# Kernel optimization log

Measured on AMD Instinct MI355X. Metric: run time of the kernel, lower is better.

Reference implementation:

```python
import jax, jax.numpy as jnp
import numpy as np

B, T, D, E, L, MAXP, PRED, TOPK = 128, 2048, 256, 32, 8, 168, 168, 2
INIT_STD = 0.02


def setup_inputs() -> dict:
    key = jax.random.key(0)
    ks = jax.random.split(key, 18)
    n = jax.random.normal
    s = INIT_STD
    inp = {
        "ctx_embed": n(ks[0], (B, T, D), jnp.float32),
        "query_experts": n(ks[1], (E, MAXP, D), jnp.float32) * s,
        "query_pos": n(ks[2], (MAXP, D), jnp.float32) * s,
        "len_emb": n(ks[3], (MAXP + 1, D), jnp.float32),  # nn.Embedding table
        "latents": n(ks[4], (L, D), jnp.float32) * s,
        "w_lat_q": n(ks[5], (D, D), jnp.float32) / np.sqrt(D),
        "w_ctx_k": n(ks[6], (D, D), jnp.float32) / np.sqrt(D),
        "w_ctx_v": n(ks[7], (D, D), jnp.float32) / np.sqrt(D),
        "w_lat_out": n(ks[8], (D, D), jnp.float32) / np.sqrt(D),
        "w_step_q": n(ks[9], (D, D), jnp.float32) / np.sqrt(D),
        "w_lat_k": n(ks[10], (D, D), jnp.float32) / np.sqrt(D),
        "w_lat_v": n(ks[11], (D, D), jnp.float32) / np.sqrt(D),
        "w_step_out": n(ks[12], (D, D), jnp.float32) / np.sqrt(D),
        "gate_w1": n(ks[13], (2 * D, D), jnp.float32) / np.sqrt(2 * D),
        "gate_b1": jnp.zeros((D,), jnp.float32),
        "gate_w2": n(ks[14], (D, E), jnp.float32) / np.sqrt(D),
        "gate_b2": jnp.zeros((E,), jnp.float32),
        "pred_len": PRED,
    }
    return inp


def _sdpa_1head(q, k, v):
    # q: [B,Q,D], k/v: [B,K,D]; single-head scaled dot-product attention
    scale = jnp.asarray(q.shape[-1], q.dtype) ** -0.5
    attn = jax.nn.softmax(jnp.einsum('bqd,bkd->bqk', q, k) * scale, axis=-1)
    return jnp.einsum('bqk,bkd->bqd', attn, v)


def reference(ctx_embed, query_experts, query_pos, len_emb, latents,
              w_lat_q, w_ctx_k, w_ctx_v, w_lat_out,
              w_step_q, w_lat_k, w_lat_v, w_step_out,
              gate_w1, gate_b1, gate_w2, gate_b2, pred_len):
    Bb, Tt, Dd = ctx_embed.shape
    P = pred_len

    # step base: positional queries + pred-length embedding
    pos = query_pos[:P][None]                      # [1,P,D]
    len_vec = len_emb[P][None, None]               # [1,1,D]
    step_base = jnp.broadcast_to(pos + len_vec, (Bb, P, Dd))

    # latent <- context cross-attention
    lat = jnp.broadcast_to(latents[None], (Bb, latents.shape[0], Dd))
    q1 = lat @ w_lat_q
    k1 = ctx_embed @ w_ctx_k
    v1 = ctx_embed @ w_ctx_v
    lat_ctx = _sdpa_1head(q1, k1, v1) @ w_lat_out  # [B,L,D]

    # step <- latent cross-attention
    q2 = step_base @ w_step_q
    k2 = lat_ctx @ w_lat_k
    v2 = lat_ctx @ w_lat_v
    step_ctx = _sdpa_1head(q2, k2, v2) @ w_step_out  # [B,P,D]

    # gating MLP over [step_base, step_ctx]
    gate_inp = jnp.concatenate([step_base, step_ctx], axis=-1)  # [B,P,2D]
    h = jax.nn.gelu(gate_inp @ gate_w1 + gate_b1, approximate=False)
    logits = h @ gate_w2 + gate_b2                               # [B,P,E]

    # top-k masking + softmax (keep top-k logits, others -> -inf)
    topv = jax.lax.top_k(logits, TOPK)[0]
    kth = topv[..., -1:]
    masked = jnp.where(logits >= kth, logits, -jnp.inf)
    weights = jax.nn.softmax(masked, axis=-1)                    # [B,P,E]

    # mixture of expert queries (einsum avoids [B,P,E,D] intermediate)
    queries = jnp.einsum('bpe,epd->bpd', weights, query_experts[:, :P, :])
    return queries
```

## Files before the change

kernel.cpp:

```cpp
#include <hip/hip_runtime.h>
#include <math.h>

#define NB 128
#define NT 2048
#define ND 256
#define NE 32
#define NL 8
#define NP 168
#define SCL 0.0625f

#define OFF_QK   0
#define OFF_WVO  4096
#define OFF_WVW  69632
#define OFF_G0   135168
#define OFF_Q2S  178176
#define OFF_AV   221184
#define OFF_DEN  8609792
#define OFF_K2   8642560
#define OFF_VW   8904704

typedef __attribute__((ext_vector_type(8))) short short8b;
typedef __attribute__((ext_vector_type(4))) float f32x4;

static __device__ __forceinline__ unsigned short f2bf(float f){
  unsigned u = __float_as_uint(f);
  u += 0x7fffu + ((u >> 16) & 1u);
  return (unsigned short)(u >> 16);
}

static __device__ __forceinline__ short8b pack8(float4 lo, float4 hi){
  short8b r;
  r[0]=(short)f2bf(lo.x); r[1]=(short)f2bf(lo.y); r[2]=(short)f2bf(lo.z); r[3]=(short)f2bf(lo.w);
  r[4]=(short)f2bf(hi.x); r[5]=(short)f2bf(hi.y); r[6]=(short)f2bf(hi.z); r[7]=(short)f2bf(hi.w);
  return r;
}

__global__ __launch_bounds__(256) void preA(const float* __restrict__ latents,
    const float* __restrict__ wlq, const float* __restrict__ wck,
    const float* __restrict__ wcv, const float* __restrict__ wlo,
    const float* __restrict__ wlv, const float* __restrict__ wso,
    const float* __restrict__ gw1, const float* __restrict__ gb1,
    const float* __restrict__ qpos, const float* __restrict__ lemb,
    const float* __restrict__ wsq, float* __restrict__ ws)
{
  int bid = blockIdx.x, tid = threadIdx.x;
  if (bid < 256){
    const float* a = wcv + bid*ND;
    float acc = 0.f;
    #pragma unroll 8
    for (int k=0;k<ND;k++) acc += a[k]*wlo[k*ND+tid];
    ws[OFF_WVO + bid*ND + tid] = acc;
  } else if (bid < 256+NP){
    int p = bid-256;
    float ag = gb1[tid], aq = 0.f;
    #pragma unroll 4
    for (int j=0;j<ND;j++){
      float sb = qpos[p*ND+j] + lemb[NP*ND+j];
      ag += sb*gw1[j*ND+tid];
      aq += sb*wsq[j*ND+tid];
    }
    ws[OFF_G0  + p*ND + tid] = ag;
    ws[OFF_Q2S + p*ND + tid] = aq*SCL;
  } else if (bid < 256+NP+256){
    int d = bid-(256+NP);
    __shared__ float ck[ND];
    __shared__ float red[4][NL];
    ck[tid] = wck[d*ND + tid];
    __syncthreads();
    const float* wrow = wlq + tid*ND;
    float macc = 0.f;
    #pragma unroll 8
    for (int k4=0;k4<64;k4++){
      float4 w4 = *(const float4*)(wrow + k4*4);
      float4 c4 = *(const float4*)(ck + k4*4);
      macc += w4.x*c4.x + w4.y*c4.y + w4.z*c4.z + w4.w*c4.w;
    }
    float part[NL];
    #pragma unroll
    for (int l=0;l<NL;l++) part[l] = latents[l*ND + tid]*macc;
    #pragma unroll
    for (int m=1;m<64;m<<=1){
      #pragma unroll
      for (int l=0;l<NL;l++) part[l] += __shfl_xor(part[l], m);
    }
    if ((tid&63)==0){
      #pragma unroll
      for (int l=0;l<NL;l++) red[tid>>6][l] = part[l];
    }
    __syncthreads();
    if (tid < NL){
      float s = red[0][tid]+red[1][tid]+red[2][tid]+red[3][tid];
      ws[OFF_QK + tid*ND + d] = s*SCL;
    }
  } else {
    int dd = bid-(256+NP+256);
    __shared__ float tmp[ND];
    const float* a = wlv + dd*ND;
    float t = 0.f;
    #pragma unroll 8
    for (int k=0;k<ND;k++) t += a[k]*wso[k*ND+tid];
    tmp[tid] = t;
    __syncthreads();
    const float* gw1b = gw1 + (size_t)ND*ND;
    float acc = 0.f;
    #pragma unroll 8
    for (int m=0;m<ND;m++) acc += tmp[m]*gw1b[m*ND+tid];
    ws[OFF_WVW + dd*ND + tid] = acc;
  }
}

__global__ __launch_bounds__(256,1) void kA(const float* __restrict__ ctx, float* __restrict__ ws)
{
  __shared__ float buf[2][64*256];
  __shared__ float efull[256*8];

  int bid = blockIdx.x;
  int tid = threadIdx.x;
  int wv = tid >> 6, lane = tid & 63;
  int c = lane & 15, g = lane >> 4;
  int dq = lane;
  int rr = wv*16 + c, r7 = rr & 7;

  short8b afrag[8];
  if (c < NL){
    const float* qk = ws + OFF_QK + c*ND + g*8;
    #pragma unroll
    for (int kk=0;kk<8;kk++){
      float4 lo = *(const float4*)(qk + kk*32);
      float4 hi = *(const float4*)(qk + kk*32 + 4);
      afrag[kk] = pack8(lo, hi);
    }
  } else {
    short8b z;
    #pragma unroll
    for (int j=0;j<8;j++) z[j] = 0;
    #pragma unroll
    for (int kk=0;kk<8;kk++) afrag[kk] = z;
  }

  float av[8][4];
  float den8[8];
  #pragma unroll
  for (int l=0;l<8;l++){
    den8[l] = 0.f;
    #pragma unroll
    for (int j=0;j<4;j++) av[l][j] = 0.f;
  }

  int lofs[8];
  #pragma unroll
  for (int j=0;j<8;j++) lofs[j] = (lane ^ j) << 2;

  const float* gw = ctx + ((size_t)bid*1024 + wv*16)*ND;

#define STAGE(PBUF, GPTR) do{                                                     \
    _Pragma("unroll")                                                             \
    for (int i_=0;i_<16;i_++){                                                    \
      __builtin_amdgcn_global_load_lds(                                           \
          (const __attribute__((address_space(1))) void*)((GPTR) + i_*ND + lofs[i_&7]), \
          (__attribute__((address_space(3))) void*)((PBUF) + (wv*16+i_)*256), 16, 0, 0); \
    }                                                                             \
  }while(0)

  STAGE(&buf[0][0], gw);

  #pragma unroll 1
  for (int s=0; s<16; ++s){
    float* pc = &buf[s&1][0];
    float* pn = &buf[(s&1)^1][0];
    int sub = s & 3;
    asm volatile("s_waitcnt lgkmcnt(0)" ::: "memory");
    __builtin_amdgcn_sched_barrier(0);
    if (s < 15){
      STAGE(pn, gw + (size_t)(s+1)*64*ND);
      asm volatile("s_waitcnt vmcnt(16)" ::: "memory");
    } else {
      asm volatile("s_waitcnt vmcnt(0)" ::: "memory");
    }
    __builtin_amdgcn_sched_barrier(0);

    f32x4 acc = {0.f,0.f,0.f,0.f};
    #pragma unroll
    for (int kk=0;kk<8;kk++){
      int sA = 2*g + 8*kk;
      float4 lo = *(const float4*)(pc + rr*256 + (((sA  ) ^ r7)<<2));
      float4 hi = *(const float4*)(pc + rr*256 + (((sA+1) ^ r7)<<2));
      acc = __builtin_amdgcn_mfma_f32_16x16x32_bf16(afrag[kk], pack8(lo,hi), acc, 0, 0, 0);
    }
    if (g < 2){
      float4 ev = make_float4(__expf(acc[0]),__expf(acc[1]),__expf(acc[2]),__expf(acc[3]));
      *(float4*)&efull[(sub*64 + rr)*8 + g*4] = ev;
    }
    asm volatile("s_waitcnt lgkmcnt(0)" ::: "memory");
    __builtin_amdgcn_sched_barrier(0);

    #pragma unroll
    for (int i=0;i<16;i++){
      int tl = wv*16 + i;
      float4 c4 = *(const float4*)(pc + tl*256 + ((dq ^ (tl&7))<<2));
      const float* ep = efull + (sub*64 + tl)*8;
      float4 e0 = *(const float4*)ep;
      float4 e1 = *(const float4*)(ep+4);
      float e8[8];
      e8[0]=e0.x; e8[1]=e0.y; e8[2]=e0.z; e8[3]=e0.w;
      e8[4]=e1.x; e8[5]=e1.y; e8[6]=e1.z; e8[7]=e1.w;
      #pragma unroll
      for (int l=0;l<8;l++){
        av[l][0] += e8[l]*c4.x;
        av[l][1] += e8[l]*c4.y;
        av[l][2] += e8[l]*c4.z;
        av[l][3] += e8[l]*c4.w;
        den8[l]  += e8[l];
      }
    }

    if (sub == 3){
      int cid = bid*4 + (s>>2);
      int pi  = cid*4 + wv;
      #pragma unroll
      for (int l=0;l<8;l++){
        *(float4*)&ws[OFF_AV + ((size_t)pi*8 + l)*ND + dq*4] =
            make_float4(av[l][0],av[l][1],av[l][2],av[l][3]);
        av[l][0]=0.f; av[l][1]=0.f; av[l][2]=0.f; av[l][3]=0.f;
      }
      if (lane == 0){
        *(float4*)&ws[OFF_DEN + pi*8    ] = make_float4(den8[0],den8[1],den8[2],den8[3]);
        *(float4*)&ws[OFF_DEN + pi*8 + 4] = make_float4(den8[4],den8[5],den8[6],den8[7]);
      }
      #pragma unroll
      for (int l=0;l<8;l++) den8[l] = 0.f;
    }
  }
#undef STAGE
}

__global__ __launch_bounds__(256) void kB1(const float* __restrict__ wlk,
                                           float* __restrict__ ws)
{
  int b = blockIdx.x;
  int d = threadIdx.x;
  __shared__ float avnT[256][8];
  __shared__ float latT[256][8];

  float dent[8];
  #pragma unroll
  for (int l=0;l<8;l++) dent[l] = 0.f;
  #pragma unroll 4
  for (int j=0;j<32;j++){
    const float* dp = ws + OFF_DEN + (size_t)(b*32+j)*8;
    float4 d0 = *(const float4*)dp;
    float4 d1 = *(const float4*)(dp+4);
    dent[0]+=d0.x; dent[1]+=d0.y; dent[2]+=d0.z; dent[3]+=d0.w;
    dent[4]+=d1.x; dent[5]+=d1.y; dent[6]+=d1.z; dent[7]+=d1.w;
  }
  float av8[8];
  #pragma unroll
  for (int l=0;l<8;l++) av8[l] = 0.f;
  #pragma unroll 2
  for (int j=0;j<32;j++){
    size_t base = OFF_AV + ((size_t)(b*32+j))*8*ND + d;
    #pragma unroll
    for (int l=0;l<8;l++) av8[l] += ws[base + (size_t)l*ND];
  }
  #pragma unroll
  for (int l=0;l<8;l++) av8[l] /= dent[l];
  *(float4*)&avnT[d][0] = make_float4(av8[0],av8[1],av8[2],av8[3]);
  *(float4*)&avnT[d][4] = make_float4(av8[4],av8[5],av8[6],av8[7]);
  __syncthreads();

  float lc[8];
  #pragma unroll
  for (int l=0;l<8;l++) lc[l] = 0.f;
  #pragma unroll 8
  for (int dd=0;dd<ND;dd++){
    float w = ws[OFF_WVO + dd*ND + d];
    float4 a0 = *(const float4*)&avnT[dd][0];
    float4 a1 = *(const float4*)&avnT[dd][4];
    lc[0]+=a0.x*w; lc[1]+=a0.y*w; lc[2]+=a0.z*w; lc[3]+=a0.w*w;
    lc[4]+=a1.x*w; lc[5]+=a1.y*w; lc[6]+=a1.z*w; lc[7]+=a1.w*w;
  }
  *(float4*)&latT[d][0] = make_float4(lc[0],lc[1],lc[2],lc[3]);
  *(float4*)&latT[d][4] = make_float4(lc[4],lc[5],lc[6],lc[7]);
  __syncthreads();

  float k2a[8], vwa[8];
  #pragma unroll
  for (int l=0;l<8;l++){ k2a[l]=0.f; vwa[l]=0.f; }
  #pragma unroll 8
  for (int dd=0;dd<ND;dd++){
    float wk = wlk[dd*ND + d];
    float wvv = ws[OFF_WVW + dd*ND + d];
    float4 a0 = *(const float4*)&latT[dd][0];
    float4 a1 = *(const float4*)&latT[dd][4];
    k2a[0]+=a0.x*wk; k2a[1]+=a0.y*wk; k2a[2]+=a0.z*wk; k2a[3]+=a0.w*wk;
    k2a[4]+=a1.x*wk; k2a[5]+=a1.y*wk; k2a[6]+=a1.z*wk; k2a[7]+=a1.w*wk;
    vwa[0]+=a0.x*wvv; vwa[1]+=a0.y*wvv; vwa[2]+=a0.z*wvv; vwa[3]+=a0.w*wvv;
    vwa[4]+=a1.x*wvv; vwa[5]+=a1.y*wvv; vwa[6]+=a1.z*wvv; vwa[7]+=a1.w*wvv;
  }
  #pragma unroll
  for (int l=0;l<8;l++){
    ws[OFF_K2 + (size_t)b*8*ND + l*ND + d] = k2a[l];
    ws[OFF_VW + (size_t)b*8*ND + l*ND + d] = vwa[l];
  }
}

__global__ __launch_bounds__(256) void kB2(const float* __restrict__ ws,
    const float* __restrict__ gw2, const float* __restrict__ gb2,
    const float* __restrict__ qe, float* __restrict__ out)
{
  int bid = blockIdx.x;
  int b = bid / 6, p0 = (bid % 6)*28;
  int tid = threadIdx.x;

  __shared__ float q2h[28][260];
  __shared__ float k2s[8][260];
  __shared__ float vws[8][260];
  __shared__ float wexp[28][8];
  __shared__ float lg[28][33];
  __shared__ float4 sel[28];

  #pragma unroll
  for (int i=0;i<7;i++){
    int idx = tid + i*256;
    int r = idx >> 6, c4 = idx & 63;
    *(float4*)&q2h[r][c4*4] = *(const float4*)&ws[OFF_Q2S + (p0+r)*ND + c4*4];
  }
  #pragma unroll
  for (int i=0;i<2;i++){
    int idx = tid + i*256;
    int l = idx >> 6, c4 = idx & 63;
    *(float4*)&k2s[l][c4*4] = *(const float4*)&ws[OFF_K2 + (size_t)(b*8+l)*ND + c4*4];
    *(float4*)&vws[l][c4*4] = *(const float4*)&ws[OFF_VW + (size_t)(b*8+l)*ND + c4*4];
  }
  __syncthreads();

  {
    int pp = tid >> 3, l1 = tid & 7;
    if (pp < 28){
      float s2 = 0.f;
      #pragma unroll 8
      for (int i=0;i<64;i++){
        float4 qa = *(const float4*)&q2h[pp][4*i];
        float4 kb = *(const float4*)&k2s[l1][4*i];
        s2 += qa.x*kb.x + qa.y*kb.y + qa.z*kb.z + qa.w*kb.w;
      }
      float e2 = __expf(s2);
      float den = e2;
      den += __shfl_xor(den,1); den += __shfl_xor(den,2); den += __shfl_xor(den,4);
      wexp[pp][l1] = e2/den;
    }
  }
  __syncthreads();

  {
    float vcol[8];
    #pragma unroll
    for (int l=0;l<8;l++) vcol[l] = vws[l][tid];
    #pragma unroll 4
    for (int p=0;p<28;p++){
      float4 w0 = *(const float4*)&wexp[p][0];
      float4 w1v = *(const float4*)&wexp[p][4];
      float x = ws[OFF_G0 + (p0+p)*ND + tid]
              + w0.x*vcol[0]+w0.y*vcol[1]+w0.z*vcol[2]+w0.w*vcol[3]
              + w1v.x*vcol[4]+w1v.y*vcol[5]+w1v.z*vcol[6]+w1v.w*vcol[7];
      q2h[p][tid] = 0.5f*x*(1.f+erff(x*0.70710678118654752f));
    }
  }
  __syncthreads();

  {
    int e = tid & 31, pq = tid >> 5;
    if (pq < 7){
      float b2v = gb2[e];
      float a0=b2v, a1=b2v, a2=b2v, a3=b2v;
      for (int cc=0;cc<ND;cc+=4){
        float w20 = gw2[(cc+0)*NE + e];
        float w21 = gw2[(cc+1)*NE + e];
        float w22 = gw2[(cc+2)*NE + e];
        float w23 = gw2[(cc+3)*NE + e];
        float4 h0 = *(const float4*)&q2h[pq*4+0][cc];
        float4 h1 = *(const float4*)&q2h[pq*4+1][cc];
        float4 h2 = *(const float4*)&q2h[pq*4+2][cc];
        float4 h3 = *(const float4*)&q2h[pq*4+3][cc];
        a0 += h0.x*w20 + h0.y*w21 + h0.z*w22 + h0.w*w23;
        a1 += h1.x*w20 + h1.y*w21 + h1.z*w22 + h1.w*w23;
        a2 += h2.x*w20 + h2.y*w21 + h2.z*w22 + h2.w*w23;
        a3 += h3.x*w20 + h3.y*w21 + h3.z*w22 + h3.w*w23;
      }
      lg[pq*4+0][e] = a0;
      lg[pq*4+1][e] = a1;
      lg[pq*4+2][e] = a2;
      lg[pq*4+3][e] = a3;
    }
  }
  __syncthreads();

  if (tid < 28){
    float m1 = -1e30f, m2 = -1e30f;
    int e1 = 0, ee2 = 0;
    for (int e3=0;e3<NE;e3++){
      float v = lg[tid][e3];
      if (v > m1){ m2 = m1; ee2 = e1; m1 = v; e1 = e3; }
      else if (v > m2){ m2 = v; ee2 = e3; }
    }
    float z = __expf(m2 - m1);
    float inv = 1.f/(1.f+z);
    sel[tid] = make_float4(__int_as_float(e1), __int_as_float(ee2), inv, z*inv);
  }
  __syncthreads();

  for (int p=0;p<28;p++){
    float4 s = sel[p];
    int e1 = __float_as_int(s.x), ee2 = __float_as_int(s.y);
    float q1v = qe[((size_t)e1*NP + (p0+p))*ND + tid];
    float q2v = qe[((size_t)ee2*NP + (p0+p))*ND + tid];
    out[((size_t)b*NP + (p0+p))*ND + tid] = s.z*q1v + s.w*q2v;
  }
}

extern "C" void kernel_launch(void* const* d_in, const int* in_sizes, int n_in,
                              void* d_out, int out_size, void* d_ws, size_t ws_size,
                              hipStream_t stream)
{
  const float* ctx  = (const float*)d_in[0];
  const float* qe   = (const float*)d_in[1];
  const float* qpos = (const float*)d_in[2];
  const float* lemb = (const float*)d_in[3];
  const float* lat  = (const float*)d_in[4];
  const float* wlq  = (const float*)d_in[5];
  const float* wck  = (const float*)d_in[6];
  const float* wcv  = (const float*)d_in[7];
  const float* wlo  = (const float*)d_in[8];
  const float* wsq  = (const float*)d_in[9];
  const float* wlk  = (const float*)d_in[10];
  const float* wlv  = (const float*)d_in[11];
  const float* wso  = (const float*)d_in[12];
  const float* gw1  = (const float*)d_in[13];
  const float* gb1  = (const float*)d_in[14];
  const float* gw2  = (const float*)d_in[15];
  const float* gb2  = (const float*)d_in[16];
  float* out = (float*)d_out;
  float* ws  = (float*)d_ws;

  preA<<<256+NP+256+256, 256, 0, stream>>>(lat, wlq, wck, wcv, wlo, wlv, wso,
                                           gw1, gb1, qpos, lemb, wsq, ws);
  kA  <<<256, 256, 0, stream>>>(ctx, ws);
  kB1 <<<NB, 256, 0, stream>>>(wlk, ws);
  kB2 <<<NB*6, 256, 0, stream>>>(ws, gw2, gb2, qe, out);
}
```

Before: 165.1 us.

## Replace MFMA LDS-staged context attention with direct-load FP32 shuffle-reduced kernel

The context attention kernel no longer stages tiles into LDS with async loads and computes scores with bf16 MFMA. It now launches 8 blocks per batch, and each block has threads load rows directly from global memory. Scores are computed in FP32 with wave shuffle reductions, and per-wave partials are reduced in shared memory, so far fewer partial results are written to the workspace. kB1 is split into two blocks per batch that compute K2 and VW separately, doubling its parallelism. The intent is more occupancy and parallelism and less reduction traffic. The cost is heavy shuffle work per row and no MFMA use.

New measurement: 175.7 us. +6.4%, slower.

```diff
diff --git a/kernel.cpp b/kernel.cpp
--- a/kernel.cpp
+++ b/kernel.cpp
@@ -15,25 +15,9 @@
 #define OFF_G0   135168
 #define OFF_Q2S  178176
 #define OFF_AV   221184
-#define OFF_DEN  8609792
-#define OFF_K2   8642560
-#define OFF_VW   8904704
-
-typedef __attribute__((ext_vector_type(8))) short short8b;
-typedef __attribute__((ext_vector_type(4))) float f32x4;
-
-static __device__ __forceinline__ unsigned short f2bf(float f){
-  unsigned u = __float_as_uint(f);
-  u += 0x7fffu + ((u >> 16) & 1u);
-  return (unsigned short)(u >> 16);
-}
-
-static __device__ __forceinline__ short8b pack8(float4 lo, float4 hi){
-  short8b r;
-  r[0]=(short)f2bf(lo.x); r[1]=(short)f2bf(lo.y); r[2]=(short)f2bf(lo.z); r[3]=(short)f2bf(lo.w);
-  r[4]=(short)f2bf(hi.x); r[5]=(short)f2bf(hi.y); r[6]=(short)f2bf(hi.z); r[7]=(short)f2bf(hi.w);
-  return r;
-}
+#define OFF_DEN  2318336
+#define OFF_K2   2326528
+#define OFF_VW   2588672
 
 __global__ __launch_bounds__(256) void preA(const float* __restrict__ latents,
     const float* __restrict__ wlq, const float* __restrict__ wck,
@@ -109,161 +93,126 @@
   }
 }
 
-__global__ __launch_bounds__(256,1) void kA(const float* __restrict__ ctx, float* __restrict__ ws)
-{
-  __shared__ float buf[2][64*256];
-  __shared__ float efull[256*8];
+__global__ __launch_bounds__(256) void kA(const float* __restrict__ ctx, float* __restrict__ ws)
+{
+  __shared__ float avred[4][8][256];
+  __shared__ float denred[4][8];
 
   int bid = blockIdx.x;
+  int b = bid >> 3, sp = bid & 7;
   int tid = threadIdx.x;
   int wv = tid >> 6, lane = tid & 63;
-  int c = lane & 15, g = lane >> 4;
-  int dq = lane;
-  int rr = wv*16 + c, r7 = rr & 7;
-
-  short8b afrag[8];
-  if (c < NL){
-    const float* qk = ws + OFF_QK + c*ND + g*8;
-    #pragma unroll
-    for (int kk=0;kk<8;kk++){
-      float4 lo = *(const float4*)(qk + kk*32);
-      float4 hi = *(const float4*)(qk + kk*32 + 4);
-      afrag[kk] = pack8(lo, hi);
-    }
-  } else {
-    short8b z;
-    #pragma unroll
-    for (int j=0;j<8;j++) z[j] = 0;
-    #pragma unroll
-    for (int kk=0;kk<8;kk++) afrag[kk] = z;
-  }
-
-  float av[8][4];
+  int tr = lane >> 5, dl = lane & 31;
+
+  float4 qkf[8][2];
+  #pragma unroll
+  for (int l=0;l<8;l++){
+    qkf[l][0] = *(const float4*)&ws[OFF_QK + l*ND + dl*4];
+    qkf[l][1] = *(const float4*)&ws[OFF_QK + l*ND + 128 + dl*4];
+  }
+
+  float4 av0[8], av1[8];
   float den8[8];
   #pragma unroll
   for (int l=0;l<8;l++){
+    av0[l] = make_float4(0.f,0.f,0.f,0.f);
+    av1[l] = make_float4(0.f,0.f,0.f,0.f);
     den8[l] = 0.f;
-    #pragma unroll
-    for (int j=0;j<4;j++) av[l][j] = 0.f;
-  }
-
-  int lofs[8];
-  #pragma unroll
-  for (int j=0;j<8;j++) lofs[j] = (lane ^ j) << 2;
-
-  const float* gw = ctx + ((size_t)bid*1024 + wv*16)*ND;
-
-#define STAGE(PBUF, GPTR) do{                                                     \
-    _Pragma("unroll")                                                             \
-    for (int i_=0;i_<16;i_++){                                                    \
-      __builtin_amdgcn_global_load_lds(                                           \
-          (const __attribute__((address_space(1))) void*)((GPTR) + i_*ND + lofs[i_&7]), \
-          (__attribute__((address_space(3))) void*)((PBUF) + (wv*16+i_)*256), 16, 0, 0); \
-    }                                                                             \
-  }while(0)
-
-  STAGE(&buf[0][0], gw);
-
-  #pragma unroll 1
-  for (int s=0; s<16; ++s){
-    float* pc = &buf[s&1][0];
-    float* pn = &buf[(s&1)^1][0];
-    int sub = s & 3;
-    asm volatile("s_waitcnt lgkmcnt(0)" ::: "memory");
-    __builtin_amdgcn_sched_barrier(0);
-    if (s < 15){
-      STAGE(pn, gw + (size_t)(s+1)*64*ND);
-      asm volatile("s_waitcnt vmcnt(16)" ::: "memory");
-    } else {
-      asm volatile("s_waitcnt vmcnt(0)" ::: "memory");
-    }
-    __builtin_amdgcn_sched_barrier(0);
-
-    f32x4 acc = {0.f,0.f,0.f,0.f};
-    #pragma unroll
-    for (int kk=0;kk<8;kk++){
-      int sA = 2*g + 8*kk;
-      float4 lo = *(const float4*)(pc + rr*256 + (((sA  ) ^ r7)<<2));
-      float4 hi = *(const float4*)(pc + rr*256 + (((sA+1) ^ r7)<<2));
-      acc = __builtin_amdgcn_mfma_f32_16x16x32_bf16(afrag[kk], pack8(lo,hi), acc, 0, 0, 0);
-    }
-    if (g < 2){
-      float4 ev = make_float4(__expf(acc[0]),__expf(acc[1]),__expf(acc[2]),__expf(acc[3]));
-      *(float4*)&efull[(sub*64 + rr)*8 + g*4] = ev;
-    }
-    asm volatile("s_waitcnt lgkmcnt(0)" ::: "memory");
-    __builtin_amdgcn_sched_barrier(0);
-
-    #pragma unroll
-    for (int i=0;i<16;i++){
-      int tl = wv*16 + i;
-      float4 c4 = *(const float4*)(pc + tl*256 + ((dq ^ (tl&7))<<2));
-      const float* ep = efull + (sub*64 + tl)*8;
-      float4 e0 = *(const float4*)ep;
-      float4 e1 = *(const float4*)(ep+4);
-      float e8[8];
-      e8[0]=e0.x; e8[1]=e0.y; e8[2]=e0.z; e8[3]=e0.w;
-      e8[4]=e1.x; e8[5]=e1.y; e8[6]=e1.z; e8[7]=e1.w;
+  }
+
+  const float* rbase = ctx + ((size_t)(b*NT + sp*256 + wv*64 + tr))*ND + dl*4;
+
+  #pragma unroll 2
+  for (int it=0; it<32; ++it){
+    const float* rp = rbase + (size_t)it*2*ND;
+    float4 f0 = *(const float4*)rp;
+    float4 f1 = *(const float4*)(rp + 128);
+    float s[8];
+    #pragma unroll
+    for (int l=0;l<8;l++){
+      s[l] = f0.x*qkf[l][0].x + f0.y*qkf[l][0].y + f0.z*qkf[l][0].z + f0.w*qkf[l][0].w
+           + f1.x*qkf[l][1].x + f1.y*qkf[l][1].y + f1.z*qkf[l][1].z + f1.w*qkf[l][1].w;
+    }
+    #pragma unroll
+    for (int m=1;m<32;m<<=1){
       #pragma unroll
-      for (int l=0;l<8;l++){
-        av[l][0] += e8[l]*c4.x;
-        av[l][1] += e8[l]*c4.y;
-        av[l][2] += e8[l]*c4.z;
-        av[l][3] += e8[l]*c4.w;
-        den8[l]  += e8[l];
-      }
-    }
-
-    if (sub == 3){
-      int cid = bid*4 + (s>>2);
-      int pi  = cid*4 + wv;
-      #pragma unroll
-      for (int l=0;l<8;l++){
-        *(float4*)&ws[OFF_AV + ((size_t)pi*8 + l)*ND + dq*4] =
-            make_float4(av[l][0],av[l][1],av[l][2],av[l][3]);
-        av[l][0]=0.f; av[l][1]=0.f; av[l][2]=0.f; av[l][3]=0.f;
-      }
-      if (lane == 0){
-        *(float4*)&ws[OFF_DEN + pi*8    ] = make_float4(den8[0],den8[1],den8[2],den8[3]);
-        *(float4*)&ws[OFF_DEN + pi*8 + 4] = make_float4(den8[4],den8[5],den8[6],den8[7]);
-      }
-      #pragma unroll
-      for (int l=0;l<8;l++) den8[l] = 0.f;
-    }
-  }
-#undef STAGE
+      for (int l=0;l<8;l++) s[l] += __shfl_xor(s[l], m);
+    }
+    #pragma unroll
+    for (int l=0;l<8;l++){
+      float e = __expf(s[l]);
+      den8[l] += e;
+      av0[l].x += e*f0.x; av0[l].y += e*f0.y; av0[l].z += e*f0.z; av0[l].w += e*f0.w;
+      av1[l].x += e*f1.x; av1[l].y += e*f1.y; av1[l].z += e*f1.z; av1[l].w += e*f1.w;
+    }
+  }
+
+  #pragma unroll
+  for (int l=0;l<8;l++){
+    av0[l].x += __shfl_xor(av0[l].x, 32); av0[l].y += __shfl_xor(av0[l].y, 32);
+    av0[l].z += __shfl_xor(av0[l].z, 32); av0[l].w += __shfl_xor(av0[l].w, 32);
+    av1[l].x += __shfl_xor(av1[l].x, 32); av1[l].y += __shfl_xor(av1[l].y, 32);
+    av1[l].z += __shfl_xor(av1[l].z, 32); av1[l].w += __shfl_xor(av1[l].w, 32);
+    den8[l] += __shfl_xor(den8[l], 32);
+  }
+
+  if (tr == 0){
+    #pragma unroll
+    for (int l=0;l<8;l++){
+      *(float4*)&avred[wv][l][dl*4]       = av0[l];
+      *(float4*)&avred[wv][l][128 + dl*4] = av1[l];
+    }
+  }
+  if (lane == 0){
+    #pragma unroll
+    for (int l=0;l<8;l++) denred[wv][l] = den8[l];
+  }
+  __syncthreads();
+
+  #pragma unroll
+  for (int rep=0; rep<2; ++rep){
+    int idx = tid + rep*256;
+    int l = idx >> 6, d4 = idx & 63;
+    float4 s0 = *(const float4*)&avred[0][l][d4*4];
+    float4 s1 = *(const float4*)&avred[1][l][d4*4];
+    float4 s2 = *(const float4*)&avred[2][l][d4*4];
+    float4 s3 = *(const float4*)&avred[3][l][d4*4];
+    float4 o;
+    o.x = s0.x+s1.x+s2.x+s3.x;
+    o.y = s0.y+s1.y+s2.y+s3.y;
+    o.z = s0.z+s1.z+s2.z+s3.z;
+    o.w = s0.w+s1.w+s2.w+s3.w;
+    *(float4*)&ws[OFF_AV + ((size_t)(bid*8 + l))*ND + d4*4] = o;
+  }
+  if (tid < NL)
+    ws[OFF_DEN + bid*8 + tid] = denred[0][tid]+denred[1][tid]+denred[2][tid]+denred[3][tid];
 }
 
 __global__ __launch_bounds__(256) void kB1(const float* __restrict__ wlk,
                                            float* __restrict__ ws)
 {
-  int b = blockIdx.x;
+  int bid = blockIdx.x;
+  int b = bid >> 1, half = bid & 1;
   int d = threadIdx.x;
   __shared__ float avnT[256][8];
   __shared__ float latT[256][8];
 
   float dent[8];
   #pragma unroll
-  for (int l=0;l<8;l++) dent[l] = 0.f;
-  #pragma unroll 4
-  for (int j=0;j<32;j++){
-    const float* dp = ws + OFF_DEN + (size_t)(b*32+j)*8;
-    float4 d0 = *(const float4*)dp;
-    float4 d1 = *(const float4*)(dp+4);
-    dent[0]+=d0.x; dent[1]+=d0.y; dent[2]+=d0.z; dent[3]+=d0.w;
-    dent[4]+=d1.x; dent[5]+=d1.y; dent[6]+=d1.z; dent[7]+=d1.w;
+  for (int l=0;l<8;l++){
+    float s = 0.f;
+    #pragma unroll
+    for (int sp=0;sp<8;sp++) s += ws[OFF_DEN + (b*8+sp)*8 + l];
+    dent[l] = s;
   }
   float av8[8];
   #pragma unroll
-  for (int l=0;l<8;l++) av8[l] = 0.f;
-  #pragma unroll 2
-  for (int j=0;j<32;j++){
-    size_t base = OFF_AV + ((size_t)(b*32+j))*8*ND + d;
-    #pragma unroll
-    for (int l=0;l<8;l++) av8[l] += ws[base + (size_t)l*ND];
-  }
-  #pragma unroll
-  for (int l=0;l<8;l++) av8[l] /= dent[l];
+  for (int l=0;l<8;l++){
+    float s = 0.f;
+    #pragma unroll
+    for (int sp=0;sp<8;sp++) s += ws[OFF_AV + ((size_t)((b*8+sp)*8 + l))*ND + d];
+    av8[l] = s / dent[l];
+  }
   *(float4*)&avnT[d][0] = make_float4(av8[0],av8[1],av8[2],av8[3]);
   *(float4*)&avnT[d][4] = make_float4(av8[4],av8[5],av8[6],av8[7]);
   __syncthreads();
@@ -283,25 +232,21 @@
   *(float4*)&latT[d][4] = make_float4(lc[4],lc[5],lc[6],lc[7]);
   __syncthreads();
 
-  float k2a[8], vwa[8];
-  #pragma unroll
-  for (int l=0;l<8;l++){ k2a[l]=0.f; vwa[l]=0.f; }
+  const float* w3 = half ? (ws + OFF_WVW) : wlk;
+  float o8[8];
+  #pragma unroll
+  for (int l=0;l<8;l++) o8[l] = 0.f;
   #pragma unroll 8
   for (int dd=0;dd<ND;dd++){
-    float wk = wlk[dd*ND + d];
-    float wvv = ws[OFF_WVW + dd*ND + d];
+    float w = w3[dd*ND + d];
     float4 a0 = *(const float4*)&latT[dd][0];
     float4 a1 = *(const float4*)&latT[dd][4];
-    k2a[0]+=a0.x*wk; k2a[1]+=a0.y*wk; k2a[2]+=a0.z*wk; k2a[3]+=a0.w*wk;
-    k2a[4]+=a1.x*wk; k2a[5]+=a1.y*wk; k2a[6]+=a1.z*wk; k2a[7]+=a1.w*wk;
-    vwa[0]+=a0.x*wvv; vwa[1]+=a0.y*wvv; vwa[2]+=a0.z*wvv; vwa[3]+=a0.w*wvv;
-    vwa[4]+=a1.x*wvv; vwa[5]+=a1.y*wvv; vwa[6]+=a1.z*wvv; vwa[7]+=a1.w*wvv;
-  }
-  #pragma unroll
-  for (int l=0;l<8;l++){
-    ws[OFF_K2 + (size_t)b*8*ND + l*ND + d] = k2a[l];
-    ws[OFF_VW + (size_t)b*8*ND + l*ND + d] = vwa[l];
-  }
+    o8[0]+=a0.x*w; o8[1]+=a0.y*w; o8[2]+=a0.z*w; o8[3]+=a0.w*w;
+    o8[4]+=a1.x*w; o8[5]+=a1.y*w; o8[6]+=a1.z*w; o8[7]+=a1.w*w;
+  }
+  size_t obase = (half ? OFF_VW : OFF_K2) + (size_t)b*8*ND + d;
+  #pragma unroll
+  for (int l=0;l<8;l++) ws[obase + l*ND] = o8[l];
 }
 
 __global__ __launch_bounds__(256) void kB2(const float* __restrict__ ws,
@@ -444,7 +389,7 @@
 
   preA<<<256+NP+256+256, 256, 0, stream>>>(lat, wlq, wck, wcv, wlo, wlv, wso,
                                            gw1, gb1, qpos, lemb, wsq, ws);
-  kA  <<<256, 256, 0, stream>>>(ctx, ws);
-  kB1 <<<NB, 256, 0, stream>>>(wlk, ws);
+  kA  <<<NB*8, 256, 0, stream>>>(ctx, ws);
+  kB1 <<<NB*2, 256, 0, stream>>>(wlk, ws);
   kB2 <<<NB*6, 256, 0, stream>>>(ws, gw2, gb2, qe, out);
 }
```
